# Optimization experiments

Hardware: AMD Instinct MI355X
Metric: run time of the kernel (lower is better)

The kernel has to match this reference:

```python
import jax, jax.numpy as jnp
import numpy as np

N = 4096
F_IN = 8
H = 64


def setup_inputs() -> dict:
    key = jax.random.key(0)
    ks = jax.random.split(key, 12)
    s_in = 1.0 / np.sqrt(F_IN)
    s_h = 1.0 / np.sqrt(2 * H)
    inp = {
        "node_features": jax.random.normal(ks[0], (N, F_IN), dtype=jnp.float32),
        "adjacency_matrix": jax.random.uniform(ks[1], (N, N), dtype=jnp.float32),
        # nn.Linear weights are (out, in)
        "W_enc": jax.random.uniform(ks[2], (H, F_IN), jnp.float32, -s_in, s_in),
        "b_enc": jax.random.uniform(ks[3], (H,), jnp.float32, -s_in, s_in),
        "W1": jax.random.uniform(ks[4], (H, 2 * H), jnp.float32, -s_h, s_h),
        "b1": jax.random.uniform(ks[5], (H,), jnp.float32, -s_h, s_h),
        "W2": jax.random.uniform(ks[6], (H, 2 * H), jnp.float32, -s_h, s_h),
        "b2": jax.random.uniform(ks[7], (H,), jnp.float32, -s_h, s_h),
        "W3": jax.random.uniform(ks[8], (H, 2 * H), jnp.float32, -s_h, s_h),
        "b3": jax.random.uniform(ks[9], (H,), jnp.float32, -s_h, s_h),
        "W_edge": jax.random.uniform(ks[10], (1, 2 * H), jnp.float32, -s_h, s_h),
        "b_edge": jax.random.uniform(ks[11], (1,), jnp.float32, -s_h, s_h),
    }
    return inp


def reference(node_features, adjacency_matrix, W_enc, b_enc, W1, b1, W2, b2, W3, b3, W_edge, b_edge):
    h = jax.nn.relu(node_features @ W_enc.T + b_enc)  # [N, H]
    for W, b in ((W1, b1), (W2, b2), (W3, b3)):
        h_neighbors = adjacency_matrix @ h            # [N, H]
        h_concat = jnp.concatenate([h, h_neighbors], axis=-1)  # [N, 2H]
        h = jax.nn.relu(h_concat @ W.T + b)
    # edge_scorer is linear: score[i,j] = w_i . h[i] + w_j . h[j] + b  (rank-1 decomposition,
    # avoids materializing the [N,N,2H] pairwise concat of the original double loop)
    w_i = W_edge[0, :H]   # [H]
    w_j = W_edge[0, H:]   # [H]
    s_i = h @ w_i         # [N]
    s_j = h @ w_j         # [N]
    scores = s_i[:, None] + s_j[None, :] + b_edge[0]  # [N, N]
    n = node_features.shape[0]
    scores = scores * (1.0 - jnp.eye(n, dtype=scores.dtype))  # diagonal stays 0
    return scores
```

## Files before the change

### kernel.cpp

```cpp
#include <hip/hip_runtime.h>

#define GN 4096
#define KS 8

typedef __attribute__((ext_vector_type(8))) short bf16x8_t;
typedef __attribute__((ext_vector_type(4))) float f32x4_t;

__device__ __forceinline__ unsigned rne(unsigned u) {
    return u + 0x7fffu + ((u >> 16) & 1u);
}
__device__ __forceinline__ unsigned pkbf(float x, float y) {
    union { float f; unsigned u; } a, b; a.f = x; b.f = y;
    return (rne(a.u) >> 16) | (rne(b.u) & 0xffff0000u);
}
__device__ __forceinline__ bf16x8_t cvt8(float4 a0, float4 a1) {
    union { unsigned u[4]; bf16x8_t v; } r;
    r.u[0] = pkbf(a0.x, a0.y);
    r.u[1] = pkbf(a0.z, a0.w);
    r.u[2] = pkbf(a1.x, a1.y);
    r.u[3] = pkbf(a1.z, a1.w);
    return r.v;
}
__device__ __forceinline__ short f2bf(float x) {
    union { float f; unsigned u; } c; c.f = x;
    return (short)(rne(c.u) >> 16);
}
__device__ __forceinline__ float bf2f(short s) {
    union { unsigned u; float f; } c; c.u = ((unsigned)(unsigned short)s) << 16;
    return c.f;
}
__device__ __forceinline__ void split8(float4 a0, float4 a1, bf16x8_t& hi, bf16x8_t& lo) {
    float v[8] = {a0.x, a0.y, a0.z, a0.w, a1.x, a1.y, a1.z, a1.w};
    union { short s[8]; bf16x8_t t; } H, L;
    #pragma unroll
    for (int i = 0; i < 8; ++i) {
        short h = f2bf(v[i]);
        H.s[i] = h;
        L.s[i] = f2bf(v[i] - bf2f(h));
    }
    hi = H.t; lo = L.t;
}
__device__ __forceinline__ void split8p(const float* p, bf16x8_t& hi, bf16x8_t& lo) {
    split8(*(const float4*)p, *(const float4*)(p + 4), hi, lo);
}

__global__ __launch_bounds__(256) void encoder_k(
    const float* __restrict__ X, const float* __restrict__ Wenc,
    const float* __restrict__ benc, float* __restrict__ h,
    short* __restrict__ Ht)
{
    const int g = blockIdx.x * 256 + threadIdx.x;
    const int i = g >> 6, f = g & 63;
    const float4 x0 = *(const float4*)(X + i * 8);
    const float4 x1 = *(const float4*)(X + i * 8 + 4);
    const float4 w0 = *(const float4*)(Wenc + f * 8);
    const float4 w1 = *(const float4*)(Wenc + f * 8 + 4);
    float acc = benc[f]
              + x0.x * w0.x + x0.y * w0.y + x0.z * w0.z + x0.w * w0.w
              + x1.x * w1.x + x1.y * w1.y + x1.z * w1.z + x1.w * w1.w;
    acc = fmaxf(acc, 0.f);
    h[g] = acc;
    Ht[f * GN + i] = f2bf(acc);
}

__global__ __launch_bounds__(256) void gemm_ah(
    const float* __restrict__ A, const short* __restrict__ Ht,
    float* __restrict__ part, int ks_len)
{
    const int t = threadIdx.x;
    const int w = t >> 6, lane = t & 63;
    const int quad = lane >> 4, l16 = lane & 15;
    const int m0 = (blockIdx.y << 6) + (w << 4);
    const int kb = blockIdx.x * ks_len;

    const float* aP = A  + (size_t)(m0 + l16) * GN + kb + quad * 8;
    const short* bP = Ht + (size_t)l16 * GN + kb + quad * 8;

    f32x4_t acc0 = {0.f, 0.f, 0.f, 0.f};
    f32x4_t acc1 = acc0, acc2 = acc0, acc3 = acc0;

    #pragma unroll 4
    for (int kk = 0; kk < ks_len; kk += 32) {
        float4   a0 = *(const float4*)(aP + kk);
        float4   a1 = *(const float4*)(aP + kk + 4);
        bf16x8_t b0 = *(const bf16x8_t*)(bP + kk);
        bf16x8_t b1 = *(const bf16x8_t*)(bP + kk + 16 * GN);
        bf16x8_t b2 = *(const bf16x8_t*)(bP + kk + 32 * GN);
        bf16x8_t b3 = *(const bf16x8_t*)(bP + kk + 48 * GN);
        bf16x8_t af = cvt8(a0, a1);
        acc0 = __builtin_amdgcn_mfma_f32_16x16x32_bf16(af, b0, acc0, 0, 0, 0);
        acc1 = __builtin_amdgcn_mfma_f32_16x16x32_bf16(af, b1, acc1, 0, 0, 0);
        acc2 = __builtin_amdgcn_mfma_f32_16x16x32_bf16(af, b2, acc2, 0, 0, 0);
        acc3 = __builtin_amdgcn_mfma_f32_16x16x32_bf16(af, b3, acc3, 0, 0, 0);
    }

    float* o = part + ((size_t)blockIdx.x * GN + m0 + quad * 4) * 64 + l16;
    #pragma unroll
    for (int r = 0; r < 4; ++r) {
        o[r * 64 +  0] = acc0[r];
        o[r * 64 + 16] = acc1[r];
        o[r * 64 + 32] = acc2[r];
        o[r * 64 + 48] = acc3[r];
    }
}

__global__ __launch_bounds__(64) void dense_split(
    const float* __restrict__ hin, const float* __restrict__ part,
    const float* __restrict__ W, const float* __restrict__ bias,
    float* __restrict__ hout, short* __restrict__ HtOut)
{
    const int lane = threadIdx.x & 63;
    const int quad = lane >> 4, l16 = lane & 15;
    const int m0 = blockIdx.x << 4;

    f32x4_t acc0 = {0.f, 0.f, 0.f, 0.f};
    f32x4_t acc1 = acc0, acc2 = acc0, acc3 = acc0;

    #pragma unroll
    for (int half = 0; half < 2; ++half) {
        #pragma unroll
        for (int kk = 0; kk < 64; kk += 32) {
            const int kq = kk + quad * 8;
            bf16x8_t ah, al;
            if (half == 0) {
                split8p(hin + (size_t)(m0 + l16) * 64 + kq, ah, al);
            } else {
                const size_t base = (size_t)(m0 + l16) * 64 + kq;
                float4 s0 = make_float4(0.f, 0.f, 0.f, 0.f);
                float4 s1 = make_float4(0.f, 0.f, 0.f, 0.f);
                #pragma unroll
                for (int p = 0; p < KS; ++p) {
                    const float* pp = part + (size_t)p * (GN * 64) + base;
                    float4 v0 = *(const float4*)pp;
                    float4 v1 = *(const float4*)(pp + 4);
                    s0.x += v0.x; s0.y += v0.y; s0.z += v0.z; s0.w += v0.w;
                    s1.x += v1.x; s1.y += v1.y; s1.z += v1.z; s1.w += v1.w;
                }
                split8(s0, s1, ah, al);
            }
            const float* wp = W + half * 64 + kq;
            bf16x8_t bh0, bl0, bh1, bl1, bh2, bl2, bh3, bl3;
            split8p(wp + (size_t)(l16     ) * 128, bh0, bl0);
            split8p(wp + (size_t)(l16 + 16) * 128, bh1, bl1);
            split8p(wp + (size_t)(l16 + 32) * 128, bh2, bl2);
            split8p(wp + (size_t)(l16 + 48) * 128, bh3, bl3);
            acc0 = __builtin_amdgcn_mfma_f32_16x16x32_bf16(ah, bh0, acc0, 0, 0, 0);
            acc0 = __builtin_amdgcn_mfma_f32_16x16x32_bf16(ah, bl0, acc0, 0, 0, 0);
            acc0 = __builtin_amdgcn_mfma_f32_16x16x32_bf16(al, bh0, acc0, 0, 0, 0);
            acc1 = __builtin_amdgcn_mfma_f32_16x16x32_bf16(ah, bh1, acc1, 0, 0, 0);
            acc1 = __builtin_amdgcn_mfma_f32_16x16x32_bf16(ah, bl1, acc1, 0, 0, 0);
            acc1 = __builtin_amdgcn_mfma_f32_16x16x32_bf16(al, bh1, acc1, 0, 0, 0);
            acc2 = __builtin_amdgcn_mfma_f32_16x16x32_bf16(ah, bh2, acc2, 0, 0, 0);
            acc2 = __builtin_amdgcn_mfma_f32_16x16x32_bf16(ah, bl2, acc2, 0, 0, 0);
            acc2 = __builtin_amdgcn_mfma_f32_16x16x32_bf16(al, bh2, acc2, 0, 0, 0);
            acc3 = __builtin_amdgcn_mfma_f32_16x16x32_bf16(ah, bh3, acc3, 0, 0, 0);
            acc3 = __builtin_amdgcn_mfma_f32_16x16x32_bf16(ah, bl3, acc3, 0, 0, 0);
            acc3 = __builtin_amdgcn_mfma_f32_16x16x32_bf16(al, bh3, acc3, 0, 0, 0);
        }
    }

    const float bia0 = bias[l16], bia1 = bias[l16 + 16];
    const float bia2 = bias[l16 + 32], bia3 = bias[l16 + 48];
    #pragma unroll
    for (int r = 0; r < 4; ++r) {
        const int node = m0 + quad * 4 + r;
        float v0 = fmaxf(acc0[r] + bia0, 0.f);
        float v1 = fmaxf(acc1[r] + bia1, 0.f);
        float v2 = fmaxf(acc2[r] + bia2, 0.f);
        float v3 = fmaxf(acc3[r] + bia3, 0.f);
        float* hp = hout + (size_t)node * 64 + l16;
        hp[ 0] = v0; hp[16] = v1; hp[32] = v2; hp[48] = v3;
        HtOut[(size_t)(l16     ) * GN + node] = f2bf(v0);
        HtOut[(size_t)(l16 + 16) * GN + node] = f2bf(v1);
        HtOut[(size_t)(l16 + 32) * GN + node] = f2bf(v2);
        HtOut[(size_t)(l16 + 48) * GN + node] = f2bf(v3);
    }
}

__global__ __launch_bounds__(256) void edge_k(
    const float* __restrict__ h, const float* __restrict__ Wedge,
    float* __restrict__ s_i, float* __restrict__ s_j)
{
    const int t = threadIdx.x;
    const int node = blockIdx.x * 4 + (t >> 6);
    const int f = t & 63;
    const float hv = h[(size_t)node * 64 + f];
    float vi = hv * Wedge[f];
    float vj = hv * Wedge[64 + f];
    #pragma unroll
    for (int off = 32; off > 0; off >>= 1) {
        vi += __shfl_xor(vi, off, 64);
        vj += __shfl_xor(vj, off, 64);
    }
    if (f == 0) { s_i[node] = vi; s_j[node] = vj; }
}

__global__ __launch_bounds__(256) void scores_k(
    const float* __restrict__ s_i, const float* __restrict__ s_j,
    const float* __restrict__ be, float* __restrict__ out)
{
    const int i  = blockIdx.y;
    const int j0 = (blockIdx.x * 256 + threadIdx.x) * 4;
    const float si = s_i[i] + be[0];
    const float4 sj = *(const float4*)(s_j + j0);
    float4 o = make_float4(si + sj.x, si + sj.y, si + sj.z, si + sj.w);
    const int d = i - j0;
    if (d >= 0 && d < 4) (&o.x)[d] = 0.f;
    *(float4*)(out + (size_t)i * GN + j0) = o;
}

extern "C" void kernel_launch(void* const* d_in, const int* in_sizes, int n_in,
                              void* d_out, int out_size, void* d_ws, size_t ws_size,
                              hipStream_t stream) {
    const float* X     = (const float*)d_in[0];
    const float* A     = (const float*)d_in[1];
    const float* Wenc  = (const float*)d_in[2];
    const float* benc  = (const float*)d_in[3];
    const float* Wmat[3] = {(const float*)d_in[4], (const float*)d_in[6], (const float*)d_in[8]};
    const float* bvec[3] = {(const float*)d_in[5], (const float*)d_in[7], (const float*)d_in[9]};
    const float* Wedge = (const float*)d_in[10];
    const float* bedge = (const float*)d_in[11];
    float* out = (float*)d_out;

    char* ws = (char*)d_ws;
    float* part = (float*)ws;
    float* h    = (float*)(ws + ((size_t)8 << 20));
    short* Ht   = (short*)(ws + ((size_t)9 << 20));
    float* s_i  = (float*)(ws + ((size_t)9 << 20) + (512u << 10));
    float* s_j  = s_i + GN;

    encoder_k<<<dim3(GN * 64 / 256), 256, 0, stream>>>(X, Wenc, benc, h, Ht);

    for (int r = 0; r < 3; ++r) {
        gemm_ah<<<dim3(KS, GN / 64), 256, 0, stream>>>(A, Ht, part, GN / KS);
        dense_split<<<dim3(GN / 16), 64, 0, stream>>>(
            h, part, Wmat[r], bvec[r], h, Ht);
    }

    edge_k<<<dim3(GN / 4), 256, 0, stream>>>(h, Wedge, s_i, s_j);
    scores_k<<<dim3(GN / 1024, GN), 256, 0, stream>>>(s_i, s_j, bedge, out);
}
```

Measured before the change: 233.5 us.

## Fuse pipeline into cooperative kernel and pre-convert adjacency to bf16 once

Replaces the encoder, the three gemm/dense launch pairs and the edge kernel with one cooperative kernel that separates stages with grid-wide syncs. At the start it converts the fp32 adjacency matrix to a bf16 copy, so the three aggregation GEMMs read half as many bytes per pass. The K split drops from 8 to 4. The trade-offs are an extra full read and write of A up front, only 256 blocks running the GEMMs, and the cost of the grid syncs.

```diff
diff --git a/kernel.cpp b/kernel.cpp
--- a/kernel.cpp
+++ b/kernel.cpp
@@ -1,7 +1,13 @@
 #include <hip/hip_runtime.h>
-
-#define GN 4096
-#define KS 8
+#include <hip/hip_cooperative_groups.h>
+
+namespace cg = cooperative_groups;
+
+#define GN   4096
+#define KS   4
+#define NBLK 256
+#define NTHR (NBLK * 256)
+#define NWAVE (NBLK * 4)
 
 typedef __attribute__((ext_vector_type(8))) short bf16x8_t;
 typedef __attribute__((ext_vector_type(4))) float f32x4_t;
@@ -44,155 +50,151 @@
     split8(*(const float4*)p, *(const float4*)(p + 4), hi, lo);
 }
 
-__global__ __launch_bounds__(256) void encoder_k(
-    const float* __restrict__ X, const float* __restrict__ Wenc,
-    const float* __restrict__ benc, float* __restrict__ h,
-    short* __restrict__ Ht)
+__global__ __launch_bounds__(256) void fused_k(
+    const float* __restrict__ X, const float* __restrict__ A,
+    const float* __restrict__ Wenc, const float* __restrict__ benc,
+    const float* __restrict__ W1, const float* __restrict__ b1,
+    const float* __restrict__ W2, const float* __restrict__ b2,
+    const float* __restrict__ W3, const float* __restrict__ b3,
+    const float* __restrict__ Wedge,
+    float* __restrict__ part, short* __restrict__ Abf,
+    float* __restrict__ h, short* __restrict__ Ht,
+    float* __restrict__ s_i, float* __restrict__ s_j)
 {
-    const int g = blockIdx.x * 256 + threadIdx.x;
-    const int i = g >> 6, f = g & 63;
-    const float4 x0 = *(const float4*)(X + i * 8);
-    const float4 x1 = *(const float4*)(X + i * 8 + 4);
-    const float4 w0 = *(const float4*)(Wenc + f * 8);
-    const float4 w1 = *(const float4*)(Wenc + f * 8 + 4);
-    float acc = benc[f]
-              + x0.x * w0.x + x0.y * w0.y + x0.z * w0.z + x0.w * w0.w
-              + x1.x * w1.x + x1.y * w1.y + x1.z * w1.z + x1.w * w1.w;
-    acc = fmaxf(acc, 0.f);
-    h[g] = acc;
-    Ht[f * GN + i] = f2bf(acc);
-}
-
-__global__ __launch_bounds__(256) void gemm_ah(
-    const float* __restrict__ A, const short* __restrict__ Ht,
-    float* __restrict__ part, int ks_len)
-{
-    const int t = threadIdx.x;
-    const int w = t >> 6, lane = t & 63;
-    const int quad = lane >> 4, l16 = lane & 15;
-    const int m0 = (blockIdx.y << 6) + (w << 4);
-    const int kb = blockIdx.x * ks_len;
-
-    const float* aP = A  + (size_t)(m0 + l16) * GN + kb + quad * 8;
-    const short* bP = Ht + (size_t)l16 * GN + kb + quad * 8;
-
-    f32x4_t acc0 = {0.f, 0.f, 0.f, 0.f};
-    f32x4_t acc1 = acc0, acc2 = acc0, acc3 = acc0;
-
-    #pragma unroll 4
-    for (int kk = 0; kk < ks_len; kk += 32) {
-        float4   a0 = *(const float4*)(aP + kk);
-        float4   a1 = *(const float4*)(aP + kk + 4);
-        bf16x8_t b0 = *(const bf16x8_t*)(bP + kk);
-        bf16x8_t b1 = *(const bf16x8_t*)(bP + kk + 16 * GN);
-        bf16x8_t b2 = *(const bf16x8_t*)(bP + kk + 32 * GN);
-        bf16x8_t b3 = *(const bf16x8_t*)(bP + kk + 48 * GN);
-        bf16x8_t af = cvt8(a0, a1);
-        acc0 = __builtin_amdgcn_mfma_f32_16x16x32_bf16(af, b0, acc0, 0, 0, 0);
-        acc1 = __builtin_amdgcn_mfma_f32_16x16x32_bf16(af, b1, acc1, 0, 0, 0);
-        acc2 = __builtin_amdgcn_mfma_f32_16x16x32_bf16(af, b2, acc2, 0, 0, 0);
-        acc3 = __builtin_amdgcn_mfma_f32_16x16x32_bf16(af, b3, acc3, 0, 0, 0);
-    }
-
-    float* o = part + ((size_t)blockIdx.x * GN + m0 + quad * 4) * 64 + l16;
-    #pragma unroll
-    for (int r = 0; r < 4; ++r) {
-        o[r * 64 +  0] = acc0[r];
-        o[r * 64 + 16] = acc1[r];
-        o[r * 64 + 32] = acc2[r];
-        o[r * 64 + 48] = acc3[r];
-    }
-}
-
-__global__ __launch_bounds__(64) void dense_split(
-    const float* __restrict__ hin, const float* __restrict__ part,
-    const float* __restrict__ W, const float* __restrict__ bias,
-    float* __restrict__ hout, short* __restrict__ HtOut)
-{
+    cg::grid_group grid = cg::this_grid();
+    const int tid  = blockIdx.x * 256 + threadIdx.x;
+    const int wid  = blockIdx.x * 4 + (threadIdx.x >> 6);
     const int lane = threadIdx.x & 63;
     const int quad = lane >> 4, l16 = lane & 15;
-    const int m0 = blockIdx.x << 4;
-
-    f32x4_t acc0 = {0.f, 0.f, 0.f, 0.f};
-    f32x4_t acc1 = acc0, acc2 = acc0, acc3 = acc0;
-
-    #pragma unroll
-    for (int half = 0; half < 2; ++half) {
+
+    for (int g = tid; g < GN * 64; g += NTHR) {
+        const int i = g >> 6, f = g & 63;
+        const float4 x0 = *(const float4*)(X + i * 8);
+        const float4 x1 = *(const float4*)(X + i * 8 + 4);
+        const float4 w0 = *(const float4*)(Wenc + f * 8);
+        const float4 w1 = *(const float4*)(Wenc + f * 8 + 4);
+        float acc = benc[f]
+                  + x0.x * w0.x + x0.y * w0.y + x0.z * w0.z + x0.w * w0.w
+                  + x1.x * w1.x + x1.y * w1.y + x1.z * w1.z + x1.w * w1.w;
+        acc = fmaxf(acc, 0.f);
+        h[g] = acc;
+        Ht[f * GN + i] = f2bf(acc);
+    }
+    #pragma unroll 4
+    for (int g = tid; g < GN * GN / 8; g += NTHR) {
+        const size_t base = (size_t)g * 8;
+        float4 a0 = *(const float4*)(A + base);
+        float4 a1 = *(const float4*)(A + base + 4);
+        *(bf16x8_t*)(Abf + base) = cvt8(a0, a1);
+    }
+    __threadfence();
+    grid.sync();
+
+    for (int r = 0; r < 3; ++r) {
+        const float* Wr = (r == 0) ? W1 : (r == 1) ? W2 : W3;
+        const float* br = (r == 0) ? b1 : (r == 1) ? b2 : b3;
+
+        {
+            const int ks = wid >> 8;
+            const int m0 = (wid & 255) << 4;
+            const int kb = ks * (GN / KS);
+
+            const short* aP = Abf + (size_t)(m0 + l16) * GN + kb + quad * 8;
+            const short* bP = Ht  + (size_t)l16 * GN + kb + quad * 8;
+
+            f32x4_t acc0 = {0.f, 0.f, 0.f, 0.f};
+            f32x4_t acc1 = acc0, acc2 = acc0, acc3 = acc0;
+
+            #pragma unroll 4
+            for (int kk = 0; kk < GN / KS; kk += 32) {
+                bf16x8_t af  = *(const bf16x8_t*)(aP + kk);
+                bf16x8_t b0v = *(const bf16x8_t*)(bP + kk);
+                bf16x8_t b1v = *(const bf16x8_t*)(bP + kk + 16 * GN);
+                bf16x8_t b2v = *(const bf16x8_t*)(bP + kk + 32 * GN);
+                bf16x8_t b3v = *(const bf16x8_t*)(bP + kk + 48 * GN);
+                acc0 = __builtin_amdgcn_mfma_f32_16x16x32_bf16(af, b0v, acc0, 0, 0, 0);
+                acc1 = __builtin_amdgcn_mfma_f32_16x16x32_bf16(af, b1v, acc1, 0, 0, 0);
+                acc2 = __builtin_amdgcn_mfma_f32_16x16x32_bf16(af, b2v, acc2, 0, 0, 0);
+                acc3 = __builtin_amdgcn_mfma_f32_16x16x32_bf16(af, b3v, acc3, 0, 0, 0);
+            }
+            float* o = part + ((size_t)ks * GN + m0 + quad * 4) * 64 + l16;
+            #pragma unroll
+            for (int rr = 0; rr < 4; ++rr) {
+                o[rr * 64 +  0] = acc0[rr];
+                o[rr * 64 + 16] = acc1[rr];
+                o[rr * 64 + 32] = acc2[rr];
+                o[rr * 64 + 48] = acc3[rr];
+            }
+        }
+        __threadfence();
+        grid.sync();
+
+        if (wid < 256) {
+            const int m0 = wid << 4;
+            f32x4_t acc[4];
+            #pragma unroll
+            for (int n = 0; n < 4; ++n) acc[n] = (f32x4_t){0.f, 0.f, 0.f, 0.f};
+
+            #pragma unroll
+            for (int half = 0; half < 2; ++half) {
+                #pragma unroll
+                for (int kk = 0; kk < 64; kk += 32) {
+                    const int kq = kk + quad * 8;
+                    bf16x8_t ah, al;
+                    if (half == 0) {
+                        split8p(h + (size_t)(m0 + l16) * 64 + kq, ah, al);
+                    } else {
+                        const size_t base = (size_t)(m0 + l16) * 64 + kq;
+                        float4 s0 = make_float4(0.f, 0.f, 0.f, 0.f);
+                        float4 s1 = make_float4(0.f, 0.f, 0.f, 0.f);
+                        #pragma unroll
+                        for (int p = 0; p < KS; ++p) {
+                            const float* pp = part + (size_t)p * (GN * 64) + base;
+                            float4 v0 = *(const float4*)pp;
+                            float4 v1 = *(const float4*)(pp + 4);
+                            s0.x += v0.x; s0.y += v0.y; s0.z += v0.z; s0.w += v0.w;
+                            s1.x += v1.x; s1.y += v1.y; s1.z += v1.z; s1.w += v1.w;
+                        }
+                        split8(s0, s1, ah, al);
+                    }
+                    const float* wp = Wr + half * 64 + kq;
+                    #pragma unroll
+                    for (int n = 0; n < 4; ++n) {
+                        bf16x8_t bh, bl;
+                        split8p(wp + (size_t)(l16 + 16 * n) * 128, bh, bl);
+                        acc[n] = __builtin_amdgcn_mfma_f32_16x16x32_bf16(ah, bh, acc[n], 0, 0, 0);
+                        acc[n] = __builtin_amdgcn_mfma_f32_16x16x32_bf16(ah, bl, acc[n], 0, 0, 0);
+                        acc[n] = __builtin_amdgcn_mfma_f32_16x16x32_bf16(al, bh, acc[n], 0, 0, 0);
+                    }
+                }
+            }
+            #pragma unroll
+            for (int rr = 0; rr < 4; ++rr) {
+                const int node = m0 + quad * 4 + rr;
+                float* hp = h + (size_t)node * 64 + l16;
+                #pragma unroll
+                for (int n = 0; n < 4; ++n) {
+                    float v = fmaxf(acc[n][rr] + br[l16 + 16 * n], 0.f);
+                    hp[16 * n] = v;
+                    if (r < 2) Ht[(size_t)(l16 + 16 * n) * GN + node] = f2bf(v);
+                }
+            }
+        }
+        __threadfence();
+        grid.sync();
+    }
+
+    for (int node = wid; node < GN; node += NWAVE) {
+        const float hv = h[(size_t)node * 64 + lane];
+        float vi = hv * Wedge[lane];
+        float vj = hv * Wedge[64 + lane];
         #pragma unroll
-        for (int kk = 0; kk < 64; kk += 32) {
-            const int kq = kk + quad * 8;
-            bf16x8_t ah, al;
-            if (half == 0) {
-                split8p(hin + (size_t)(m0 + l16) * 64 + kq, ah, al);
-            } else {
-                const size_t base = (size_t)(m0 + l16) * 64 + kq;
-                float4 s0 = make_float4(0.f, 0.f, 0.f, 0.f);
-                float4 s1 = make_float4(0.f, 0.f, 0.f, 0.f);
-                #pragma unroll
-                for (int p = 0; p < KS; ++p) {
-                    const float* pp = part + (size_t)p * (GN * 64) + base;
-                    float4 v0 = *(const float4*)pp;
-                    float4 v1 = *(const float4*)(pp + 4);
-                    s0.x += v0.x; s0.y += v0.y; s0.z += v0.z; s0.w += v0.w;
-                    s1.x += v1.x; s1.y += v1.y; s1.z += v1.z; s1.w += v1.w;
-                }
-                split8(s0, s1, ah, al);
-            }
-            const float* wp = W + half * 64 + kq;
-            bf16x8_t bh0, bl0, bh1, bl1, bh2, bl2, bh3, bl3;
-            split8p(wp + (size_t)(l16     ) * 128, bh0, bl0);
-            split8p(wp + (size_t)(l16 + 16) * 128, bh1, bl1);
-            split8p(wp + (size_t)(l16 + 32) * 128, bh2, bl2);
-            split8p(wp + (size_t)(l16 + 48) * 128, bh3, bl3);
-            acc0 = __builtin_amdgcn_mfma_f32_16x16x32_bf16(ah, bh0, acc0, 0, 0, 0);
-            acc0 = __builtin_amdgcn_mfma_f32_16x16x32_bf16(ah, bl0, acc0, 0, 0, 0);
-            acc0 = __builtin_amdgcn_mfma_f32_16x16x32_bf16(al, bh0, acc0, 0, 0, 0);
-            acc1 = __builtin_amdgcn_mfma_f32_16x16x32_bf16(ah, bh1, acc1, 0, 0, 0);
-            acc1 = __builtin_amdgcn_mfma_f32_16x16x32_bf16(ah, bl1, acc1, 0, 0, 0);
-            acc1 = __builtin_amdgcn_mfma_f32_16x16x32_bf16(al, bh1, acc1, 0, 0, 0);
-            acc2 = __builtin_amdgcn_mfma_f32_16x16x32_bf16(ah, bh2, acc2, 0, 0, 0);
-            acc2 = __builtin_amdgcn_mfma_f32_16x16x32_bf16(ah, bl2, acc2, 0, 0, 0);
-            acc2 = __builtin_amdgcn_mfma_f32_16x16x32_bf16(al, bh2, acc2, 0, 0, 0);
-            acc3 = __builtin_amdgcn_mfma_f32_16x16x32_bf16(ah, bh3, acc3, 0, 0, 0);
-            acc3 = __builtin_amdgcn_mfma_f32_16x16x32_bf16(ah, bl3, acc3, 0, 0, 0);
-            acc3 = __builtin_amdgcn_mfma_f32_16x16x32_bf16(al, bh3, acc3, 0, 0, 0);
+        for (int off = 32; off > 0; off >>= 1) {
+            vi += __shfl_xor(vi, off, 64);
+            vj += __shfl_xor(vj, off, 64);
         }
-    }
-
-    const float bia0 = bias[l16], bia1 = bias[l16 + 16];
-    const float bia2 = bias[l16 + 32], bia3 = bias[l16 + 48];
-    #pragma unroll
-    for (int r = 0; r < 4; ++r) {
-        const int node = m0 + quad * 4 + r;
-        float v0 = fmaxf(acc0[r] + bia0, 0.f);
-        float v1 = fmaxf(acc1[r] + bia1, 0.f);
-        float v2 = fmaxf(acc2[r] + bia2, 0.f);
-        float v3 = fmaxf(acc3[r] + bia3, 0.f);
-        float* hp = hout + (size_t)node * 64 + l16;
-        hp[ 0] = v0; hp[16] = v1; hp[32] = v2; hp[48] = v3;
-        HtOut[(size_t)(l16     ) * GN + node] = f2bf(v0);
-        HtOut[(size_t)(l16 + 16) * GN + node] = f2bf(v1);
-        HtOut[(size_t)(l16 + 32) * GN + node] = f2bf(v2);
-        HtOut[(size_t)(l16 + 48) * GN + node] = f2bf(v3);
-    }
-}
-
-__global__ __launch_bounds__(256) void edge_k(
-    const float* __restrict__ h, const float* __restrict__ Wedge,
-    float* __restrict__ s_i, float* __restrict__ s_j)
-{
-    const int t = threadIdx.x;
-    const int node = blockIdx.x * 4 + (t >> 6);
-    const int f = t & 63;
-    const float hv = h[(size_t)node * 64 + f];
-    float vi = hv * Wedge[f];
-    float vj = hv * Wedge[64 + f];
-    #pragma unroll
-    for (int off = 32; off > 0; off >>= 1) {
-        vi += __shfl_xor(vi, off, 64);
-        vj += __shfl_xor(vj, off, 64);
-    }
-    if (f == 0) { s_i[node] = vi; s_j[node] = vj; }
+        if (lane == 0) { s_i[node] = vi; s_j[node] = vj; }
+    }
 }
 
 __global__ __launch_bounds__(256) void scores_k(
@@ -216,27 +218,32 @@
     const float* A     = (const float*)d_in[1];
     const float* Wenc  = (const float*)d_in[2];
     const float* benc  = (const float*)d_in[3];
-    const float* Wmat[3] = {(const float*)d_in[4], (const float*)d_in[6], (const float*)d_in[8]};
-    const float* bvec[3] = {(const float*)d_in[5], (const float*)d_in[7], (const float*)d_in[9]};
+    const float* W1    = (const float*)d_in[4];
+    const float* b1    = (const float*)d_in[5];
+    const float* W2    = (const float*)d_in[6];
+    const float* b2    = (const float*)d_in[7];
+    const float* W3    = (const float*)d_in[8];
+    const float* b3    = (const float*)d_in[9];
     const float* Wedge = (const float*)d_in[10];
     const float* bedge = (const float*)d_in[11];
     float* out = (float*)d_out;
 
     char* ws = (char*)d_ws;
     float* part = (float*)ws;
-    float* h    = (float*)(ws + ((size_t)8 << 20));
-    short* Ht   = (short*)(ws + ((size_t)9 << 20));
-    float* s_i  = (float*)(ws + ((size_t)9 << 20) + (512u << 10));
+    short* Abf  = (short*)(ws + ((size_t)4 << 20));
+    float* h    = (float*)(ws + ((size_t)36 << 20));
+    short* Ht   = (short*)(ws + ((size_t)37 << 20));
+    float* s_i  = (float*)(ws + ((size_t)38 << 20));
     float* s_j  = s_i + GN;
 
-    encoder_k<<<dim3(GN * 64 / 256), 256, 0, stream>>>(X, Wenc, benc, h, Ht);
-
-    for (int r = 0; r < 3; ++r) {
-        gemm_ah<<<dim3(KS, GN / 64), 256, 0, stream>>>(A, Ht, part, GN / KS);
-        dense_split<<<dim3(GN / 16), 64, 0, stream>>>(
-            h, part, Wmat[r], bvec[r], h, Ht);
-    }
-
-    edge_k<<<dim3(GN / 4), 256, 0, stream>>>(h, Wedge, s_i, s_j);
+    void* args[] = {
+        (void*)&X, (void*)&A, (void*)&Wenc, (void*)&benc,
+        (void*)&W1, (void*)&b1, (void*)&W2, (void*)&b2,
+        (void*)&W3, (void*)&b3, (void*)&Wedge,
+        (void*)&part, (void*)&Abf, (void*)&h,
+        (void*)&Ht, (void*)&s_i, (void*)&s_j };
+    hipLaunchCooperativeKernel((void*)fused_k, dim3(NBLK), dim3(256),
+                               args, 0, stream);
+
     scores_k<<<dim3(GN / 1024, GN), 256, 0, stream>>>(s_i, s_j, bedge, out);
 }
```

New measurement: 674.4 us. 189% more time.
